# Kernel optimization log

Measured on AMD Instinct MI355X. Metric: run time of the kernel, lower is better.

Reference implementation:

```python
import jax, jax.numpy as jnp
import numpy as np

B, L, D = 64, 1024, 1024


def _attn(q, K, V, mask):
    # q: [B,D], K/V: [B,L,D], mask: [B,L] bool (True = valid)
    scores = jnp.einsum('bd,bld->bl', q, K) / jnp.sqrt(jnp.asarray(D, q.dtype))
    scores = jnp.where(mask, scores, -jnp.inf)
    attn = jax.nn.softmax(scores, axis=-1)
    attn = jnp.where(jnp.isnan(attn), 0.0, attn)  # torch.nan_to_num for all-masked rows
    return jnp.einsum('bl,bld->bd', attn, V)


def setup_inputs() -> dict:
    key = jax.random.key(0)
    ks = jax.random.split(key, 12)
    xav = float(np.sqrt(6.0 / (D + D)))  # xavier_uniform for square Linear
    img_mask = jax.random.randint(ks[4], (B, L), 0, 2).astype(bool)
    txt_mask = jax.random.randint(ks[7], (B, L), 0, 2).astype(bool)
    # guarantee at least one valid token per row
    img_mask = img_mask.at[:, 0].set(True)
    txt_mask = txt_mask.at[:, 0].set(True)
    return {
        'img_q': jax.random.normal(ks[0], (B, D), jnp.float32),
        'txt_q': jax.random.normal(ks[1], (B, D), jnp.float32),
        'K_img': jax.random.normal(ks[2], (B, L, D), jnp.float32),
        'V_img': jax.random.normal(ks[3], (B, L, D), jnp.float32),
        'img_mask': img_mask,
        'K_txt': jax.random.normal(ks[5], (B, L, D), jnp.float32),
        'V_txt': jax.random.normal(ks[6], (B, L, D), jnp.float32),
        'txt_mask': txt_mask,
        'W_img': jax.random.uniform(ks[8], (D, D), jnp.float32, -xav, xav),
        'b_img': jnp.zeros((D,), jnp.float32),
        'W_txt': jax.random.uniform(ks[9], (D, D), jnp.float32, -xav, xav),
        'b_txt': jnp.zeros((D,), jnp.float32),
    }


def reference(img_q, txt_q, K_img, V_img, img_mask, K_txt, V_txt, txt_mask,
              W_img, b_img, W_txt, b_txt):
    # Dropout is identity in eval mode.
    ctx_img = _attn(txt_q, K_img, V_img, img_mask)
    img_q = img_q + ctx_img @ W_img.T + b_img
    ctx_txt = _attn(img_q, K_txt, V_txt, txt_mask)
    txt_q = txt_q + ctx_txt @ W_txt.T + b_txt
    return (img_q, txt_q)
```

## Files before the change

### kernel.cpp

```cpp
#include <hip/hip_runtime.h>
#include <hip/hip_bf16.h>
#include <float.h>

#define B_ 64
#define L_ 1024
#define D_ 1024
#define NSPLIT 8
#define CHUNK 128
#define PSTRIDE 1028

typedef __bf16 bf16x8 __attribute__((ext_vector_type(8)));
typedef float f32x4 __attribute__((ext_vector_type(4)));

__device__ inline unsigned short f2bf(float x) {
    unsigned int u = __float_as_uint(x);
    unsigned int lsb = (u >> 16) & 1u;
    u += 0x7fffu + lsb;
    return (unsigned short)(u >> 16);
}

__global__ __launch_bounds__(512, 2) void attn_kernel(
    const float* __restrict__ q,
    const float* __restrict__ K,
    const float* __restrict__ V,
    const int*   __restrict__ mask,
    float* __restrict__ part,
    const float* __restrict__ cs0,
    const float* __restrict__ cs1,
    unsigned short* __restrict__ cd0,
    unsigned short* __restrict__ cd1,
    int nattn)
{
    const int tid = threadIdx.x;

    if ((int)blockIdx.x >= nattn) {
        int i = ((int)blockIdx.x - nattn) * 512 + tid;
        float4 v0 = reinterpret_cast<const float4*>(cs0)[i];
        float4 v1 = reinterpret_cast<const float4*>(cs1)[i];
        ushort4 u0, u1;
        u0.x = f2bf(v0.x); u0.y = f2bf(v0.y); u0.z = f2bf(v0.z); u0.w = f2bf(v0.w);
        u1.x = f2bf(v1.x); u1.y = f2bf(v1.y); u1.z = f2bf(v1.z); u1.w = f2bf(v1.w);
        reinterpret_cast<ushort4*>(cd0)[i] = u0;
        reinterpret_cast<ushort4*>(cd1)[i] = u1;
        return;
    }

    const int bid  = blockIdx.x;
    const int b    = bid >> 3;
    const int sp   = bid & 7;
    const int l0   = sp * CHUNK;
    const int wave = tid >> 6;
    const int lane = tid & 63;

    __shared__ int    vidx[CHUNK];
    __shared__ int    nvalid;
    __shared__ float4 ored[8 * 256];
    __shared__ float  sered[8];

    const float4* qptr = reinterpret_cast<const float4*>(q + (size_t)b * D_);
    float4 qreg[4];
    #pragma unroll
    for (int rep = 0; rep < 4; ++rep) qreg[rep] = qptr[lane + rep * 64];

    if (wave == 0) {
        const int* mp = mask + (size_t)b * L_ + l0;
        int mv0 = mp[lane];
        int mv1 = mp[64 + lane];
        unsigned long long bal0 = __ballot(mv0 != 0);
        unsigned long long bal1 = __ballot(mv1 != 0);
        int n0 = __popcll(bal0);
        int nv = n0 + __popcll(bal1);
        unsigned long long lt = (1ull << lane) - 1;
        if (mv0) vidx[__popcll(bal0 & lt)] = lane;
        if (mv1) vidx[n0 + __popcll(bal1 & lt)] = 64 + lane;
        int padv = bal0 ? (__ffsll((long long)bal0) - 1)
                        : (bal1 ? 64 + __ffsll((long long)bal1) - 1 : 0);
        if (nv + lane < CHUNK) vidx[nv + lane] = padv;
        if (lane == 0) nvalid = nv;
    }
    __syncthreads();
    const int nv    = nvalid;
    const int nvp16 = (nv + 15) & ~15;

    const float* Kb = K + ((size_t)b * L_ + l0) * D_;
    const float* Vb = V + ((size_t)b * L_ + l0) * D_;

    float4 o0 = {0,0,0,0}, o1 = {0,0,0,0}, o2 = {0,0,0,0}, o3 = {0,0,0,0};
    float se = 0.f;

    for (int j = wave; j < nvp16; j += 16) {
        int ra = vidx[j];
        int rb = vidx[j + 8];
        const float4* kra = reinterpret_cast<const float4*>(Kb + ra * D_);
        const float4* vra = reinterpret_cast<const float4*>(Vb + ra * D_);
        const float4* krb = reinterpret_cast<const float4*>(Kb + rb * D_);
        const float4* vrb = reinterpret_cast<const float4*>(Vb + rb * D_);
        float4 ka[4], va[4], kb[4], vb[4];
        #pragma unroll
        for (int rep = 0; rep < 4; ++rep) {
            ka[rep] = kra[lane + rep * 64];
            kb[rep] = krb[lane + rep * 64];
            va[rep] = vra[lane + rep * 64];
            vb[rep] = vrb[lane + rep * 64];
        }

        float sa0 = 0.f, sa1 = 0.f, sb0 = 0.f, sb1 = 0.f;
        #pragma unroll
        for (int rep = 0; rep < 4; rep += 2) {
            sa0 += ka[rep].x * qreg[rep].x + ka[rep].y * qreg[rep].y
                 + ka[rep].z * qreg[rep].z + ka[rep].w * qreg[rep].w;
            sa1 += ka[rep+1].x * qreg[rep+1].x + ka[rep+1].y * qreg[rep+1].y
                 + ka[rep+1].z * qreg[rep+1].z + ka[rep+1].w * qreg[rep+1].w;
            sb0 += kb[rep].x * qreg[rep].x + kb[rep].y * qreg[rep].y
                 + kb[rep].z * qreg[rep].z + kb[rep].w * qreg[rep].w;
            sb1 += kb[rep+1].x * qreg[rep+1].x + kb[rep+1].y * qreg[rep+1].y
                 + kb[rep+1].z * qreg[rep+1].z + kb[rep+1].w * qreg[rep+1].w;
        }
        float sA = sa0 + sa1, sB = sb0 + sb1;
        #pragma unroll
        for (int off = 32; off > 0; off >>= 1) {
            sA += __shfl_xor(sA, off, 64);
            sB += __shfl_xor(sB, off, 64);
        }

        float pA = (j     < nv) ? __expf(sA * 0.03125f) : 0.f;
        float pB = (j + 8 < nv) ? __expf(sB * 0.03125f) : 0.f;
        se += pA + pB;
        o0.x += pA * va[0].x + pB * vb[0].x;  o0.y += pA * va[0].y + pB * vb[0].y;
        o0.z += pA * va[0].z + pB * vb[0].z;  o0.w += pA * va[0].w + pB * vb[0].w;
        o1.x += pA * va[1].x + pB * vb[1].x;  o1.y += pA * va[1].y + pB * vb[1].y;
        o1.z += pA * va[1].z + pB * vb[1].z;  o1.w += pA * va[1].w + pB * vb[1].w;
        o2.x += pA * va[2].x + pB * vb[2].x;  o2.y += pA * va[2].y + pB * vb[2].y;
        o2.z += pA * va[2].z + pB * vb[2].z;  o2.w += pA * va[2].w + pB * vb[2].w;
        o3.x += pA * va[3].x + pB * vb[3].x;  o3.y += pA * va[3].y + pB * vb[3].y;
        o3.z += pA * va[3].z + pB * vb[3].z;  o3.w += pA * va[3].w + pB * vb[3].w;
    }

    ored[wave * 256 + lane      ] = o0;
    ored[wave * 256 + lane +  64] = o1;
    ored[wave * 256 + lane + 128] = o2;
    ored[wave * 256 + lane + 192] = o3;
    if (lane == 0) sered[wave] = se;
    __syncthreads();

    float* po = part + (size_t)bid * PSTRIDE;
    if (tid < 256) {
        float4 acc = ored[tid];
        #pragma unroll
        for (int w = 1; w < 8; ++w) {
            float4 v = ored[w * 256 + tid];
            acc.x += v.x; acc.y += v.y; acc.z += v.z; acc.w += v.w;
        }
        reinterpret_cast<float4*>(po)[tid] = acc;
    }
    if (tid == 0) {
        float t = 0.f;
        #pragma unroll
        for (int w = 0; w < 8; ++w) t += sered[w];
        po[D_] = t;
    }
}

__global__ __launch_bounds__(256) void combine_kernel(
    const float* __restrict__ part,
    unsigned short* __restrict__ ctxb)
{
    const int b   = blockIdx.x;
    const int tid = threadIdx.x;
    const float* pb = part + (size_t)b * NSPLIT * PSTRIDE;

    float denom = 0.f;
    #pragma unroll
    for (int s = 0; s < NSPLIT; ++s) denom += pb[(size_t)s * PSTRIDE + D_];
    float inv = 1.f / denom;

    float ax = 0.f, ay = 0.f, az = 0.f, aw = 0.f;
    #pragma unroll
    for (int s = 0; s < NSPLIT; ++s) {
        float4 o = reinterpret_cast<const float4*>(pb + (size_t)s * PSTRIDE)[tid];
        ax += o.x; ay += o.y; az += o.z; aw += o.w;
    }
    ushort4 u;
    u.x = f2bf(ax * inv); u.y = f2bf(ay * inv);
    u.z = f2bf(az * inv); u.w = f2bf(aw * inv);
    reinterpret_cast<ushort4*>(ctxb)[(size_t)b * (D_ / 4) + tid] = u;
}

__global__ __launch_bounds__(256) void proj_kernel(
    const unsigned short* __restrict__ Abf,
    const unsigned short* __restrict__ Wbf,
    const float* __restrict__ qin,
    const float* __restrict__ bias,
    float* __restrict__ out)
{
    const int tid  = threadIdx.x;
    const int wave = tid >> 6;
    const int lane = tid & 63;
    const int m0   = (blockIdx.x & 3) * 16;
    const int n0   = (blockIdx.x >> 2) * 16;
    const int r    = lane & 15;
    const int g    = lane >> 4;

    const bf16x8* aptr = reinterpret_cast<const bf16x8*>(
        Abf + (size_t)(m0 + r) * D_ + g * 8 + wave * 256);
    const bf16x8* bptr = reinterpret_cast<const bf16x8*>(
        Wbf + (size_t)(n0 + r) * D_ + g * 8 + wave * 256);

    f32x4 acc = {0.f, 0.f, 0.f, 0.f};
    #pragma unroll
    for (int kk = 0; kk < 8; ++kk) {
        bf16x8 a  = aptr[kk * 4];
        bf16x8 bb = bptr[kk * 4];
        acc = __builtin_amdgcn_mfma_f32_16x16x32_bf16(a, bb, acc, 0, 0, 0);
    }

    __shared__ float red[1024];
    #pragma unroll
    for (int i = 0; i < 4; ++i) red[wave * 256 + lane * 4 + i] = acc[i];
    __syncthreads();

    int ol = tid >> 2, oi = tid & 3;
    float v = red[ol * 4 + oi] + red[256 + ol * 4 + oi]
            + red[512 + ol * 4 + oi] + red[768 + ol * 4 + oi];
    int row = m0 + ((ol >> 4) * 4 + oi);
    int col = n0 + (ol & 15);
    out[(size_t)row * D_ + col] = qin[(size_t)row * D_ + col] + bias[col] + v;
}

extern "C" void kernel_launch(void* const* d_in, const int* in_sizes, int n_in,
                              void* d_out, int out_size, void* d_ws, size_t ws_size,
                              hipStream_t stream) {
    const float* img_q    = (const float*)d_in[0];
    const float* txt_q    = (const float*)d_in[1];
    const float* K_img    = (const float*)d_in[2];
    const float* V_img    = (const float*)d_in[3];
    const int*   img_mask = (const int*)  d_in[4];
    const float* K_txt    = (const float*)d_in[5];
    const float* V_txt    = (const float*)d_in[6];
    const int*   txt_mask = (const int*)  d_in[7];
    const float* W_img    = (const float*)d_in[8];
    const float* b_img    = (const float*)d_in[9];
    const float* W_txt    = (const float*)d_in[10];
    const float* b_txt    = (const float*)d_in[11];

    float* out_img = (float*)d_out;
    float* out_txt = (float*)d_out + B_ * D_;

    char* ws = (char*)d_ws;
    float* part = (float*)ws;
    size_t part_bytes = (size_t)B_ * NSPLIT * PSTRIDE * sizeof(float);
    unsigned short* Wimg_bf = (unsigned short*)(ws + part_bytes);
    unsigned short* Wtxt_bf = Wimg_bf + (size_t)D_ * D_;
    unsigned short* ctx_bf  = Wtxt_bf + (size_t)D_ * D_;

    attn_kernel<<<1024, 512, 0, stream>>>(
        txt_q, K_img, V_img, img_mask, part,
        W_img, W_txt, Wimg_bf, Wtxt_bf, B_ * NSPLIT);
    combine_kernel<<<B_, 256, 0, stream>>>(part, ctx_bf);
    proj_kernel<<<256, 256, 0, stream>>>(ctx_bf, Wimg_bf, img_q, b_img, out_img);
    attn_kernel<<<512, 512, 0, stream>>>(
        out_img, K_txt, V_txt, txt_mask, part,
        nullptr, nullptr, nullptr, nullptr, B_ * NSPLIT);
    combine_kernel<<<B_, 256, 0, stream>>>(part, ctx_bf);
    proj_kernel<<<256, 256, 0, stream>>>(ctx_bf, Wtxt_bf, txt_q, b_txt, out_txt);
}
```

Baseline: 123.5 us.

## Fuse split-combine into fp32 GEMV projection and drop bf16 weight conversion

After: 158.9 us. 1.29x slower.

```diff
diff --git a/kernel.cpp b/kernel.cpp
--- a/kernel.cpp
+++ b/kernel.cpp
@@ -1,5 +1,4 @@
 #include <hip/hip_runtime.h>
-#include <hip/hip_bf16.h>
 #include <float.h>
 
 #define B_ 64
@@ -9,42 +8,14 @@
 #define CHUNK 128
 #define PSTRIDE 1028
 
-typedef __bf16 bf16x8 __attribute__((ext_vector_type(8)));
-typedef float f32x4 __attribute__((ext_vector_type(4)));
-
-__device__ inline unsigned short f2bf(float x) {
-    unsigned int u = __float_as_uint(x);
-    unsigned int lsb = (u >> 16) & 1u;
-    u += 0x7fffu + lsb;
-    return (unsigned short)(u >> 16);
-}
-
 __global__ __launch_bounds__(512, 2) void attn_kernel(
     const float* __restrict__ q,
     const float* __restrict__ K,
     const float* __restrict__ V,
     const int*   __restrict__ mask,
-    float* __restrict__ part,
-    const float* __restrict__ cs0,
-    const float* __restrict__ cs1,
-    unsigned short* __restrict__ cd0,
-    unsigned short* __restrict__ cd1,
-    int nattn)
+    float* __restrict__ part)
 {
-    const int tid = threadIdx.x;
-
-    if ((int)blockIdx.x >= nattn) {
-        int i = ((int)blockIdx.x - nattn) * 512 + tid;
-        float4 v0 = reinterpret_cast<const float4*>(cs0)[i];
-        float4 v1 = reinterpret_cast<const float4*>(cs1)[i];
-        ushort4 u0, u1;
-        u0.x = f2bf(v0.x); u0.y = f2bf(v0.y); u0.z = f2bf(v0.z); u0.w = f2bf(v0.w);
-        u1.x = f2bf(v1.x); u1.y = f2bf(v1.y); u1.z = f2bf(v1.z); u1.w = f2bf(v1.w);
-        reinterpret_cast<ushort4*>(cd0)[i] = u0;
-        reinterpret_cast<ushort4*>(cd1)[i] = u1;
-        return;
-    }
-
+    const int tid  = threadIdx.x;
     const int bid  = blockIdx.x;
     const int b    = bid >> 3;
     const int sp   = bid & 7;
@@ -161,70 +132,79 @@
     }
 }
 
-__global__ __launch_bounds__(256) void combine_kernel(
+__global__ __launch_bounds__(256) void cproj_kernel(
     const float* __restrict__ part,
-    unsigned short* __restrict__ ctxb)
-{
-    const int b   = blockIdx.x;
-    const int tid = threadIdx.x;
-    const float* pb = part + (size_t)b * NSPLIT * PSTRIDE;
-
-    float denom = 0.f;
-    #pragma unroll
-    for (int s = 0; s < NSPLIT; ++s) denom += pb[(size_t)s * PSTRIDE + D_];
-    float inv = 1.f / denom;
-
-    float ax = 0.f, ay = 0.f, az = 0.f, aw = 0.f;
-    #pragma unroll
-    for (int s = 0; s < NSPLIT; ++s) {
-        float4 o = reinterpret_cast<const float4*>(pb + (size_t)s * PSTRIDE)[tid];
-        ax += o.x; ay += o.y; az += o.z; aw += o.w;
-    }
-    ushort4 u;
-    u.x = f2bf(ax * inv); u.y = f2bf(ay * inv);
-    u.z = f2bf(az * inv); u.w = f2bf(aw * inv);
-    reinterpret_cast<ushort4*>(ctxb)[(size_t)b * (D_ / 4) + tid] = u;
-}
-
-__global__ __launch_bounds__(256) void proj_kernel(
-    const unsigned short* __restrict__ Abf,
-    const unsigned short* __restrict__ Wbf,
+    const float* __restrict__ W,
     const float* __restrict__ qin,
     const float* __restrict__ bias,
     float* __restrict__ out)
 {
     const int tid  = threadIdx.x;
+    const int b    = blockIdx.x >> 3;
+    const int n0   = (blockIdx.x & 7) * 128;
     const int wave = tid >> 6;
     const int lane = tid & 63;
-    const int m0   = (blockIdx.x & 3) * 16;
-    const int n0   = (blockIdx.x >> 2) * 16;
-    const int r    = lane & 15;
-    const int g    = lane >> 4;
-
-    const bf16x8* aptr = reinterpret_cast<const bf16x8*>(
-        Abf + (size_t)(m0 + r) * D_ + g * 8 + wave * 256);
-    const bf16x8* bptr = reinterpret_cast<const bf16x8*>(
-        Wbf + (size_t)(n0 + r) * D_ + g * 8 + wave * 256);
-
-    f32x4 acc = {0.f, 0.f, 0.f, 0.f};
+
+    __shared__ float ctx[D_];
+    __shared__ float invs;
+
+    const float* pb = part + (size_t)b * NSPLIT * PSTRIDE;
+    if (tid == 0) {
+        float d = 0.f;
+        #pragma unroll
+        for (int s = 0; s < NSPLIT; ++s) d += pb[(size_t)s * PSTRIDE + D_];
+        invs = 1.f / d;
+    }
+    float4 c = {0.f, 0.f, 0.f, 0.f};
     #pragma unroll
-    for (int kk = 0; kk < 8; ++kk) {
-        bf16x8 a  = aptr[kk * 4];
-        bf16x8 bb = bptr[kk * 4];
-        acc = __builtin_amdgcn_mfma_f32_16x16x32_bf16(a, bb, acc, 0, 0, 0);
-    }
-
-    __shared__ float red[1024];
+    for (int s = 0; s < NSPLIT; ++s) {
+        float4 v = reinterpret_cast<const float4*>(pb + (size_t)s * PSTRIDE)[tid];
+        c.x += v.x; c.y += v.y; c.z += v.z; c.w += v.w;
+    }
+    __syncthreads();
+    float inv = invs;
+    c.x *= inv; c.y *= inv; c.z *= inv; c.w *= inv;
+    reinterpret_cast<float4*>(ctx)[tid] = c;
+    __syncthreads();
+
+    float4 cx[4];
     #pragma unroll
-    for (int i = 0; i < 4; ++i) red[wave * 256 + lane * 4 + i] = acc[i];
-    __syncthreads();
-
-    int ol = tid >> 2, oi = tid & 3;
-    float v = red[ol * 4 + oi] + red[256 + ol * 4 + oi]
-            + red[512 + ol * 4 + oi] + red[768 + ol * 4 + oi];
-    int row = m0 + ((ol >> 4) * 4 + oi);
-    int col = n0 + (ol & 15);
-    out[(size_t)row * D_ + col] = qin[(size_t)row * D_ + col] + bias[col] + v;
+    for (int rep = 0; rep < 4; ++rep)
+        cx[rep] = reinterpret_cast<const float4*>(ctx)[lane + rep * 64];
+
+    for (int n = wave; n < 128; n += 8) {
+        int na = n0 + n, nb = n0 + n + 4;
+        const float4* wa = reinterpret_cast<const float4*>(W + (size_t)na * D_);
+        const float4* wb = reinterpret_cast<const float4*>(W + (size_t)nb * D_);
+        float4 A[4], Bv[4];
+        #pragma unroll
+        for (int rep = 0; rep < 4; ++rep) {
+            A[rep]  = wa[lane + rep * 64];
+            Bv[rep] = wb[lane + rep * 64];
+        }
+        float a0 = 0.f, a1 = 0.f, b0 = 0.f, b1 = 0.f;
+        #pragma unroll
+        for (int rep = 0; rep < 4; rep += 2) {
+            a0 += A[rep].x * cx[rep].x + A[rep].y * cx[rep].y
+                + A[rep].z * cx[rep].z + A[rep].w * cx[rep].w;
+            a1 += A[rep+1].x * cx[rep+1].x + A[rep+1].y * cx[rep+1].y
+                + A[rep+1].z * cx[rep+1].z + A[rep+1].w * cx[rep+1].w;
+            b0 += Bv[rep].x * cx[rep].x + Bv[rep].y * cx[rep].y
+                + Bv[rep].z * cx[rep].z + Bv[rep].w * cx[rep].w;
+            b1 += Bv[rep+1].x * cx[rep+1].x + Bv[rep+1].y * cx[rep+1].y
+                + Bv[rep+1].z * cx[rep+1].z + Bv[rep+1].w * cx[rep+1].w;
+        }
+        float dA = a0 + a1, dB = b0 + b1;
+        #pragma unroll
+        for (int off = 32; off > 0; off >>= 1) {
+            dA += __shfl_xor(dA, off, 64);
+            dB += __shfl_xor(dB, off, 64);
+        }
+        if (lane == 0) {
+            out[(size_t)b * D_ + na] = qin[(size_t)b * D_ + na] + bias[na] + dA;
+            out[(size_t)b * D_ + nb] = qin[(size_t)b * D_ + nb] + bias[nb] + dB;
+        }
+    }
 }
 
 extern "C" void kernel_launch(void* const* d_in, const int* in_sizes, int n_in,
@@ -246,21 +226,12 @@
     float* out_img = (float*)d_out;
     float* out_txt = (float*)d_out + B_ * D_;
 
-    char* ws = (char*)d_ws;
-    float* part = (float*)ws;
-    size_t part_bytes = (size_t)B_ * NSPLIT * PSTRIDE * sizeof(float);
-    unsigned short* Wimg_bf = (unsigned short*)(ws + part_bytes);
-    unsigned short* Wtxt_bf = Wimg_bf + (size_t)D_ * D_;
-    unsigned short* ctx_bf  = Wtxt_bf + (size_t)D_ * D_;
-
-    attn_kernel<<<1024, 512, 0, stream>>>(
-        txt_q, K_img, V_img, img_mask, part,
-        W_img, W_txt, Wimg_bf, Wtxt_bf, B_ * NSPLIT);
-    combine_kernel<<<B_, 256, 0, stream>>>(part, ctx_bf);
-    proj_kernel<<<256, 256, 0, stream>>>(ctx_bf, Wimg_bf, img_q, b_img, out_img);
-    attn_kernel<<<512, 512, 0, stream>>>(
-        out_img, K_txt, V_txt, txt_mask, part,
-        nullptr, nullptr, nullptr, nullptr, B_ * NSPLIT);
-    combine_kernel<<<B_, 256, 0, stream>>>(part, ctx_bf);
-    proj_kernel<<<256, 256, 0, stream>>>(ctx_bf, Wtxt_bf, txt_q, b_txt, out_txt);
+    float* part = (float*)d_ws;
+
+    attn_kernel<<<B_ * NSPLIT, 512, 0, stream>>>(
+        txt_q, K_img, V_img, img_mask, part);
+    cproj_kernel<<<512, 256, 0, stream>>>(part, W_img, img_q, b_img, out_img);
+    attn_kernel<<<B_ * NSPLIT, 512, 0, stream>>>(
+        out_img, K_txt, V_txt, txt_mask, part);
+    cproj_kernel<<<512, 256, 0, stream>>>(part, W_txt, txt_q, b_txt, out_txt);
 }
```
